# Optimization experiments

Measured on AMD Instinct MI355X. Metric: run time of the kernel, lower is better.

## Reference

```python
import jax, jax.numpy as jnp
import numpy as np
from jax import lax

N, F, V = 16, 5, 4  # batch, frames, nodes-per-frame

def _maxpool3(x):
    # MaxPool2d(kernel=3, stride=3), NCHW
    return lax.reduce_window(x, -jnp.inf, lax.max, (1, 1, 3, 3), (1, 1, 3, 3), 'VALID')

def _conv(x, w, b):
    y = lax.conv_general_dilated(x, w, window_strides=(2, 2), padding='VALID',
                                 dimension_numbers=('NCHW', 'OIHW', 'NCHW'))
    return y + b[None, :, None, None]

def setup_inputs() -> dict:
    key = jax.random.key(0)
    ks = jax.random.split(key, 24)
    s = 0.05
    inp = {
        'nodes':  jax.random.normal(ks[0], (N, F, V, 3, 224, 224), jnp.float32),
        'pos':    jax.random.normal(ks[1], (N, F, V, 6), jnp.float32),
        'attmap': jax.random.uniform(ks[2], (N, F, V, V), jnp.float32),
        'depths': jax.random.normal(ks[3], (N, F, V), jnp.float32),
        # params (linear weights stored [in, out]; y = x @ W + b)
        'conv1_w': jax.random.normal(ks[4], (3, 3, 3, 3), jnp.float32) * s,
        'conv1_b': jax.random.normal(ks[5], (3,), jnp.float32) * s,
        'conv2_w': jax.random.normal(ks[6], (1, 3, 3, 3), jnp.float32) * s,
        'conv2_b': jax.random.normal(ks[7], (1,), jnp.float32) * s,
        'lin_w':   jax.random.normal(ks[8], (36, 6), jnp.float32) * s,
        'lin_b':   jax.random.normal(ks[9], (6,), jnp.float32) * s,
        'wfc_w':   jax.random.normal(ks[10], (24, 1), jnp.float32) * s,
        'wfc_b':   jax.random.normal(ks[11], (1,), jnp.float32) * s,
        'fm_w':    jax.random.normal(ks[12], (6, 6), jnp.float32) * s,
        'fm_b':    jax.random.normal(ks[13], (6,), jnp.float32) * s,
        'lm_w':    jax.random.normal(ks[14], (6, 6), jnp.float32) * s,
        'lm_b':    jax.random.normal(ks[15], (6,), jnp.float32) * s,
        'fc1_w':   jax.random.normal(ks[16], (240, 120), jnp.float32) * s,
        'fc1_b':   jax.random.normal(ks[17], (120,), jnp.float32) * s,
        'fc2_w':   jax.random.normal(ks[18], (120, 60), jnp.float32) * s,
        'fc2_b':   jax.random.normal(ks[19], (60,), jnp.float32) * s,
        'fc3_w':   jax.random.normal(ks[20], (60, 6), jnp.float32) * s,
        'fc3_b':   jax.random.normal(ks[21], (6,), jnp.float32) * s,
    }
    return inp

def reference(nodes, pos, attmap, depths,
              conv1_w, conv1_b, conv2_w, conv2_b, lin_w, lin_b,
              wfc_w, wfc_b, fm_w, fm_b, lm_w, lm_b,
              fc1_w, fc1_b, fc2_w, fc2_b, fc3_w, fc3_b):
    # --- CNN node encoder ---
    x = nodes.reshape(N * F * V, 3, 224, 224)
    h = jax.nn.relu(_maxpool3(_conv(x, conv1_w, conv1_b)))          # [B*,3,37,37]
    h = jax.nn.relu(_maxpool3(_conv(h, conv2_w, conv2_b)))          # [B*,1,6,6]
    feat = h.reshape(N, F, V, 36) @ lin_w + lin_b                    # [N,F,V,6]

    # --- edge weights: sigmoid(W . cat(feat_src, feat_tgt)) ---
    na = jnp.concatenate([feat, pos], axis=-1)                       # [N,F,V,12]
    src = jnp.broadcast_to(na[:, :, :, None, :], (N, F, V, V, 12))   # s along axis 2
    tgt = jnp.broadcast_to(na[:, :, None, :, :], (N, F, V, V, 12))   # t along axis 3
    ef = jnp.concatenate([src, tgt], axis=-1)                        # [N,F,V,V,24]
    link = jax.nn.sigmoid((ef @ wfc_w)[..., 0] + wfc_b[0])           # [N,F,s,t]

    maw = link + attmap                                              # [N,F,s,t]

    # --- attention-weighted message aggregation over source nodes ---
    pm = pos @ fm_w + fm_b                                           # [N,F,V,6]
    agg = jnp.einsum('bfsn,bfsd->bfnd', maw, pm)                     # [N,F,V,6]

    # last-frame message (frame 0 has none)
    prev = jnp.concatenate([jnp.zeros_like(pos[:, :1]), pos[:, :-1]], axis=1)
    lm = prev @ lm_w + lm_b                                          # [N,F,V,6]
    frame_mask = (jnp.arange(F) > 0)[None, :, None, None]
    pos_up = agg + jnp.where(frame_mask, lm, 0.0)

    # --- readout MLP ---
    inp = jnp.concatenate([feat, pos_up], axis=-1).reshape(N, F * V * 12)  # [N,240]
    r = jax.nn.relu(inp @ fc1_w + fc1_b)
    r = jax.nn.relu(r @ fc2_w + fc2_b)
    return r @ fc3_w + fc3_b                                         # [N,6]
```

## Files before the change

### kernel.cpp

```cpp
#include <hip/hip_runtime.h>
#include <math.h>

#define NB 16
#define NF 5
#define NV 4
#define NIMG (NB*NF*NV)
#define IMG_HW 224
#define IMG_CH_STRIDE (224*224)
#define H1_HW 37
#define H1_CH_STRIDE (37*37)
#define H1_IMG 4108
#define PB_PER_IMG 19

typedef float v4f __attribute__((ext_vector_type(4)));

__global__ __launch_bounds__(256) void k1_conv1_pool(
    const float* __restrict__ nodes,
    const float* __restrict__ w,
    const float* __restrict__ bias,
    float* __restrict__ h1)
{
    const int blk = blockIdx.x;
    const int img = blk / PB_PER_IMG;
    const int pb  = blk - img * PB_PER_IMG;
    const int t   = threadIdx.x;

    const int py0    = 2 * pb;
    const int nrows  = (pb == PB_PER_IMG - 1) ? 1 : 2;
    const int r0     = 12 * pb;
    const int nflt   = (6 * nrows + 1) * 224;
    const int nf4    = nflt >> 2;

    __shared__ float s[3 * 13 * 224];
    __shared__ float s_w[27 * 3];
    __shared__ float s_b[3];

    if (t < 81) s_w[t] = w[t];
    if (t < 3)  s_b[t] = bias[t];

    {
        const v4f* s0 = (const v4f*)(nodes + (size_t)img * 3 * IMG_CH_STRIDE + r0 * IMG_HW);
        const v4f* s1 = s0 + (IMG_CH_STRIDE >> 2);
        const v4f* s2 = s1 + (IMG_CH_STRIDE >> 2);
        v4f* d0 = (v4f*)s;
        v4f* d1 = (v4f*)(s + nflt);
        v4f* d2 = (v4f*)(s + 2 * nflt);
        for (int i = t; i < nf4; i += 256) {
            v4f a0 = __builtin_nontemporal_load(&s0[i]);
            v4f a1 = __builtin_nontemporal_load(&s1[i]);
            v4f a2 = __builtin_nontemporal_load(&s2[i]);
            d0[i] = a0; d1[i] = a1; d2[i] = a2;
        }
    }
    __syncthreads();

    if (t < 111 * nrows) {
        const int r  = (t >= 111) ? 1 : 0;
        const int u  = t - 111 * r;
        const int oc = u / 37;
        const int px = u - 37 * oc;

        float acc[9];
        #pragma unroll
        for (int p = 0; p < 9; ++p) acc[p] = 0.f;

        #pragma unroll
        for (int ic = 0; ic < 3; ++ic) {
            float wv[9];
            #pragma unroll
            for (int k = 0; k < 9; ++k) wv[k] = s_w[(oc * 3 + ic) * 9 + k];

            float patch[7][8];
            #pragma unroll
            for (int rr = 0; rr < 7; ++rr) {
                const float* row = s + ic * nflt + (6 * r + rr) * 224 + 6 * px;
                #pragma unroll
                for (int k = 0; k < 4; ++k) {
                    float2 q = *(const float2*)(row + 2 * k);
                    patch[rr][2 * k]     = q.x;
                    patch[rr][2 * k + 1] = q.y;
                }
            }

            #pragma unroll
            for (int i = 0; i < 3; ++i)
                #pragma unroll
                for (int j = 0; j < 3; ++j) {
                    const int p = i * 3 + j;
                    #pragma unroll
                    for (int ky = 0; ky < 3; ++ky)
                        #pragma unroll
                        for (int kx = 0; kx < 3; ++kx)
                            acc[p] += wv[ky * 3 + kx] * patch[2 * i + ky][2 * j + kx];
                }
        }

        float m = -INFINITY;
        #pragma unroll
        for (int p = 0; p < 9; ++p) m = fmaxf(m, acc[p]);
        m += s_b[oc];
        m = fmaxf(m, 0.f);
        h1[(size_t)img * H1_IMG + oc * H1_CH_STRIDE + (py0 + r) * H1_HW + px] = m;
    }
}

__global__ __launch_bounds__(128) void k2_conv2_pool_lin(
    const float* __restrict__ h1,
    const float* __restrict__ w2,
    const float* __restrict__ b2,
    const float* __restrict__ lin_w,
    const float* __restrict__ lin_b,
    float* __restrict__ feat)
{
    const int img = blockIdx.x;
    const int t   = threadIdx.x;
    __shared__ float s[H1_IMG];
    __shared__ float s_h2[36];

    {
        const float4* src = (const float4*)(h1 + (size_t)img * H1_IMG);
        float4* d = (float4*)s;
        float4 v[8];
        #pragma unroll
        for (int k = 0; k < 8; ++k) v[k] = src[t + 128 * k];
        const bool hi = (t < 1027 - 1024);
        float4 v8;
        if (hi) v8 = src[t + 1024];
        #pragma unroll
        for (int k = 0; k < 8; ++k) d[t + 128 * k] = v[k];
        if (hi) d[t + 1024] = v8;
    }
    __syncthreads();

    if (t < 36) {
        const int py = t / 6, px = t - (t / 6) * 6;
        float m = -INFINITY;
        #pragma unroll
        for (int i = 0; i < 3; ++i)
            #pragma unroll
            for (int j = 0; j < 3; ++j) {
                const int oy = 3 * py + i, ox = 3 * px + j;
                float a = 0.f;
                #pragma unroll
                for (int ic = 0; ic < 3; ++ic)
                    #pragma unroll
                    for (int ky = 0; ky < 3; ++ky)
                        #pragma unroll
                        for (int kx = 0; kx < 3; ++kx)
                            a += w2[(ic * 3 + ky) * 3 + kx] *
                                 s[ic * H1_CH_STRIDE + (2 * oy + ky) * H1_HW + (2 * ox + kx)];
                m = fmaxf(m, a);
            }
        m += b2[0];
        s_h2[t] = fmaxf(m, 0.f);
    }
    __syncthreads();
    if (t < 6) {
        float a = lin_b[t];
        #pragma unroll
        for (int i = 0; i < 36; ++i) a += s_h2[i] * lin_w[i * 6 + t];
        feat[img * 6 + t] = a;
    }
}

__global__ __launch_bounds__(128) void k3_graph_mlp(
    const float* __restrict__ feat,
    const float* __restrict__ pos,
    const float* __restrict__ attmap,
    const float* __restrict__ wfc_w,
    const float* __restrict__ wfc_b,
    const float* __restrict__ fm_w,
    const float* __restrict__ fm_b,
    const float* __restrict__ lm_w,
    const float* __restrict__ lm_b,
    const float* __restrict__ fc1_w,
    const float* __restrict__ fc1_b,
    const float* __restrict__ fc2_w,
    const float* __restrict__ fc2_b,
    const float* __restrict__ fc3_w,
    const float* __restrict__ fc3_b,
    float* __restrict__ out)
{
    const int b = blockIdx.x;
    const int t = threadIdx.x;

    __shared__ float s_na[NF][NV][12];
    __shared__ float s_pm[NF][NV][6];
    __shared__ float s_maw[NF][NV][NV];
    __shared__ float s_inp[240];
    __shared__ float s_r1[120];
    __shared__ float s_r2[60];

    if (t < 120) {
        int f = t / 24;
        int v = (t / 6) % 4;
        int d = t % 6;
        float fv = feat[((b * NF + f) * NV + v) * 6 + d];
        float pv = pos[((b * NF + f) * NV + v) * 6 + d];
        s_na[f][v][d]     = fv;
        s_na[f][v][6 + d] = pv;
        s_inp[(f * NV + v) * 12 + d] = fv;
    }
    __syncthreads();

    if (t < 120) {
        int f = t / 24;
        int v = (t / 6) % 4;
        int d = t % 6;
        float a = fm_b[d];
        #pragma unroll
        for (int k = 0; k < 6; ++k) a += s_na[f][v][6 + k] * fm_w[k * 6 + d];
        s_pm[f][v][d] = a;
    }
    if (t < 80) {
        int f = t / 16;
        int sidx = (t / 4) % 4;
        int tt = t % 4;
        float x = wfc_b[0];
        #pragma unroll
        for (int k = 0; k < 12; ++k)
            x += wfc_w[k] * s_na[f][sidx][k] + wfc_w[12 + k] * s_na[f][tt][k];
        float sig = 1.f / (1.f + expf(-x));
        s_maw[f][sidx][tt] = sig + attmap[((b * NF + f) * NV + sidx) * NV + tt];
    }
    __syncthreads();

    if (t < 120) {
        int f = t / 24;
        int n = (t / 6) % 4;
        int d = t % 6;
        float a = 0.f;
        #pragma unroll
        for (int sidx = 0; sidx < 4; ++sidx) a += s_maw[f][sidx][n] * s_pm[f][sidx][d];
        if (f > 0) {
            float l = lm_b[d];
            #pragma unroll
            for (int k = 0; k < 6; ++k) l += s_na[f - 1][n][6 + k] * lm_w[k * 6 + d];
            a += l;
        }
        s_inp[(f * NV + n) * 12 + 6 + d] = a;
    }
    __syncthreads();

    if (t < 120) {
        float a = fc1_b[t];
        #pragma unroll 16
        for (int i = 0; i < 240; ++i) a += s_inp[i] * fc1_w[i * 120 + t];
        s_r1[t] = fmaxf(a, 0.f);
    }
    __syncthreads();

    if (t < 60) {
        float a = fc2_b[t];
        #pragma unroll 16
        for (int i = 0; i < 120; ++i) a += s_r1[i] * fc2_w[i * 60 + t];
        s_r2[t] = fmaxf(a, 0.f);
    }
    __syncthreads();

    if (t < 6) {
        float a = fc3_b[t];
        #pragma unroll 12
        for (int i = 0; i < 60; ++i) a += s_r2[i] * fc3_w[i * 6 + t];
        out[b * 6 + t] = a;
    }
}

extern "C" void kernel_launch(void* const* d_in, const int* in_sizes, int n_in,
                              void* d_out, int out_size, void* d_ws, size_t ws_size,
                              hipStream_t stream) {
    const float* nodes   = (const float*)d_in[0];
    const float* pos     = (const float*)d_in[1];
    const float* attmap  = (const float*)d_in[2];
    const float* conv1_w = (const float*)d_in[4];
    const float* conv1_b = (const float*)d_in[5];
    const float* conv2_w = (const float*)d_in[6];
    const float* conv2_b = (const float*)d_in[7];
    const float* lin_w   = (const float*)d_in[8];
    const float* lin_b   = (const float*)d_in[9];
    const float* wfc_w   = (const float*)d_in[10];
    const float* wfc_b   = (const float*)d_in[11];
    const float* fm_w    = (const float*)d_in[12];
    const float* fm_b    = (const float*)d_in[13];
    const float* lm_w    = (const float*)d_in[14];
    const float* lm_b    = (const float*)d_in[15];
    const float* fc1_w   = (const float*)d_in[16];
    const float* fc1_b   = (const float*)d_in[17];
    const float* fc2_w   = (const float*)d_in[18];
    const float* fc2_b   = (const float*)d_in[19];
    const float* fc3_w   = (const float*)d_in[20];
    const float* fc3_b   = (const float*)d_in[21];

    float* h1      = (float*)d_ws;
    float* feat_ws = h1 + (size_t)NIMG * H1_IMG;

    k1_conv1_pool<<<NIMG * PB_PER_IMG, 256, 0, stream>>>(nodes, conv1_w, conv1_b, h1);
    k2_conv2_pool_lin<<<NIMG, 128, 0, stream>>>(h1, conv2_w, conv2_b, lin_w, lin_b, feat_ws);
    k3_graph_mlp<<<NB, 128, 0, stream>>>(feat_ws, pos, attmap,
                                         wfc_w, wfc_b, fm_w, fm_b, lm_w, lm_b,
                                         fc1_w, fc1_b, fc2_w, fc2_b, fc3_w, fc3_b,
                                         (float*)d_out);
}
```

Baseline: 321.2 us.

## Compute all conv1 channels per thread, 3 pooled rows per block, fuse conv2 into graph kernel

Result: slower. 343.1 us (+6.8%).

```diff
diff --git a/kernel.cpp b/kernel.cpp
--- a/kernel.cpp
+++ b/kernel.cpp
@@ -10,7 +10,7 @@
 #define H1_HW 37
 #define H1_CH_STRIDE (37*37)
 #define H1_IMG 4108
-#define PB_PER_IMG 19
+#define PB_PER_IMG 13
 
 typedef float v4f __attribute__((ext_vector_type(4)));
 
@@ -25,18 +25,14 @@
     const int pb  = blk - img * PB_PER_IMG;
     const int t   = threadIdx.x;
 
-    const int py0    = 2 * pb;
-    const int nrows  = (pb == PB_PER_IMG - 1) ? 1 : 2;
-    const int r0     = 12 * pb;
+    const int last   = (pb == PB_PER_IMG - 1);
+    const int py0    = 3 * pb;
+    const int nrows  = last ? 1 : 3;
+    const int r0     = 18 * pb;
     const int nflt   = (6 * nrows + 1) * 224;
     const int nf4    = nflt >> 2;
 
-    __shared__ float s[3 * 13 * 224];
-    __shared__ float s_w[27 * 3];
-    __shared__ float s_b[3];
-
-    if (t < 81) s_w[t] = w[t];
-    if (t < 3)  s_b[t] = bias[t];
+    __shared__ float s[3 * 19 * 224];
 
     {
         const v4f* s0 = (const v4f*)(nodes + (size_t)img * 3 * IMG_CH_STRIDE + r0 * IMG_HW);
@@ -54,21 +50,24 @@
     }
     __syncthreads();
 
-    if (t < 111 * nrows) {
-        const int r  = (t >= 111) ? 1 : 0;
-        const int u  = t - 111 * r;
-        const int oc = u / 37;
-        const int px = u - 37 * oc;
-
-        float acc[9];
-        #pragma unroll
-        for (int p = 0; p < 9; ++p) acc[p] = 0.f;
+    if (t < H1_HW * nrows) {
+        const int r  = t / H1_HW;
+        const int px = t - H1_HW * r;
+
+        float acc[3][9];
+        #pragma unroll
+        for (int oc = 0; oc < 3; ++oc)
+            #pragma unroll
+            for (int p = 0; p < 9; ++p) acc[oc][p] = 0.f;
 
         #pragma unroll
         for (int ic = 0; ic < 3; ++ic) {
-            float wv[9];
-            #pragma unroll
-            for (int k = 0; k < 9; ++k) wv[k] = s_w[(oc * 3 + ic) * 9 + k];
+            float wv[3][9];
+            #pragma unroll
+            for (int oc = 0; oc < 3; ++oc)
+                #pragma unroll
+                for (int k = 0; k < 9; ++k)
+                    wv[oc][k] = w[(oc * 3 + ic) * 9 + k];
 
             float patch[7][8];
             #pragma unroll
@@ -90,81 +89,34 @@
                     #pragma unroll
                     for (int ky = 0; ky < 3; ++ky)
                         #pragma unroll
-                        for (int kx = 0; kx < 3; ++kx)
-                            acc[p] += wv[ky * 3 + kx] * patch[2 * i + ky][2 * j + kx];
+                        for (int kx = 0; kx < 3; ++kx) {
+                            float x = patch[2 * i + ky][2 * j + kx];
+                            acc[0][p] += wv[0][ky * 3 + kx] * x;
+                            acc[1][p] += wv[1][ky * 3 + kx] * x;
+                            acc[2][p] += wv[2][ky * 3 + kx] * x;
+                        }
                 }
         }
 
-        float m = -INFINITY;
-        #pragma unroll
-        for (int p = 0; p < 9; ++p) m = fmaxf(m, acc[p]);
-        m += s_b[oc];
-        m = fmaxf(m, 0.f);
-        h1[(size_t)img * H1_IMG + oc * H1_CH_STRIDE + (py0 + r) * H1_HW + px] = m;
+        float* outb = h1 + (size_t)img * H1_IMG + (py0 + r) * H1_HW + px;
+        #pragma unroll
+        for (int oc = 0; oc < 3; ++oc) {
+            float m = -INFINITY;
+            #pragma unroll
+            for (int p = 0; p < 9; ++p) m = fmaxf(m, acc[oc][p]);
+            m += bias[oc];
+            m = fmaxf(m, 0.f);
+            outb[oc * H1_CH_STRIDE] = m;
+        }
     }
 }
 
-__global__ __launch_bounds__(128) void k2_conv2_pool_lin(
+__global__ __launch_bounds__(256) void k23_feat_graph_mlp(
     const float* __restrict__ h1,
     const float* __restrict__ w2,
     const float* __restrict__ b2,
     const float* __restrict__ lin_w,
     const float* __restrict__ lin_b,
-    float* __restrict__ feat)
-{
-    const int img = blockIdx.x;
-    const int t   = threadIdx.x;
-    __shared__ float s[H1_IMG];
-    __shared__ float s_h2[36];
-
-    {
-        const float4* src = (const float4*)(h1 + (size_t)img * H1_IMG);
-        float4* d = (float4*)s;
-        float4 v[8];
-        #pragma unroll
-        for (int k = 0; k < 8; ++k) v[k] = src[t + 128 * k];
-        const bool hi = (t < 1027 - 1024);
-        float4 v8;
-        if (hi) v8 = src[t + 1024];
-        #pragma unroll
-        for (int k = 0; k < 8; ++k) d[t + 128 * k] = v[k];
-        if (hi) d[t + 1024] = v8;
-    }
-    __syncthreads();
-
-    if (t < 36) {
-        const int py = t / 6, px = t - (t / 6) * 6;
-        float m = -INFINITY;
-        #pragma unroll
-        for (int i = 0; i < 3; ++i)
-            #pragma unroll
-            for (int j = 0; j < 3; ++j) {
-                const int oy = 3 * py + i, ox = 3 * px + j;
-                float a = 0.f;
-                #pragma unroll
-                for (int ic = 0; ic < 3; ++ic)
-                    #pragma unroll
-                    for (int ky = 0; ky < 3; ++ky)
-                        #pragma unroll
-                        for (int kx = 0; kx < 3; ++kx)
-                            a += w2[(ic * 3 + ky) * 3 + kx] *
-                                 s[ic * H1_CH_STRIDE + (2 * oy + ky) * H1_HW + (2 * ox + kx)];
-                m = fmaxf(m, a);
-            }
-        m += b2[0];
-        s_h2[t] = fmaxf(m, 0.f);
-    }
-    __syncthreads();
-    if (t < 6) {
-        float a = lin_b[t];
-        #pragma unroll
-        for (int i = 0; i < 36; ++i) a += s_h2[i] * lin_w[i * 6 + t];
-        feat[img * 6 + t] = a;
-    }
-}
-
-__global__ __launch_bounds__(128) void k3_graph_mlp(
-    const float* __restrict__ feat,
     const float* __restrict__ pos,
     const float* __restrict__ attmap,
     const float* __restrict__ wfc_w,
@@ -184,6 +136,10 @@
     const int b = blockIdx.x;
     const int t = threadIdx.x;
 
+    __shared__ float s[5 * H1_IMG];
+    __shared__ float s_h2[5][36];
+    __shared__ float s_feat[20][6];
+
     __shared__ float s_na[NF][NV][12];
     __shared__ float s_pm[NF][NV][6];
     __shared__ float s_maw[NF][NV][NV];
@@ -191,11 +147,57 @@
     __shared__ float s_r1[120];
     __shared__ float s_r2[60];
 
+    for (int ph = 0; ph < 4; ++ph) {
+        const int img0 = b * 20 + ph * 5;
+        {
+            const float4* src = (const float4*)(h1 + (size_t)img0 * H1_IMG);
+            float4* d = (float4*)s;
+            for (int i = t; i < 5 * 1027; i += 256) d[i] = src[i];
+        }
+        __syncthreads();
+
+        if (t < 180) {
+            const int im = t / 36;
+            const int u  = t - im * 36;
+            const int py = u / 6, px = u - (u / 6) * 6;
+            const float* si = s + im * H1_IMG;
+            float m = -INFINITY;
+            #pragma unroll
+            for (int i = 0; i < 3; ++i)
+                #pragma unroll
+                for (int j = 0; j < 3; ++j) {
+                    const int oy = 3 * py + i, ox = 3 * px + j;
+                    float a = 0.f;
+                    #pragma unroll
+                    for (int ic = 0; ic < 3; ++ic)
+                        #pragma unroll
+                        for (int ky = 0; ky < 3; ++ky)
+                            #pragma unroll
+                            for (int kx = 0; kx < 3; ++kx)
+                                a += w2[(ic * 3 + ky) * 3 + kx] *
+                                     si[ic * H1_CH_STRIDE + (2 * oy + ky) * H1_HW + (2 * ox + kx)];
+                    m = fmaxf(m, a);
+                }
+            m += b2[0];
+            s_h2[im][u] = fmaxf(m, 0.f);
+        }
+        __syncthreads();
+
+        if (t < 30) {
+            const int im = t / 6, d = t - (t / 6) * 6;
+            float a = lin_b[d];
+            #pragma unroll
+            for (int i = 0; i < 36; ++i) a += s_h2[im][i] * lin_w[i * 6 + d];
+            s_feat[ph * 5 + im][d] = a;
+        }
+        __syncthreads();
+    }
+
     if (t < 120) {
         int f = t / 24;
         int v = (t / 6) % 4;
         int d = t % 6;
-        float fv = feat[((b * NF + f) * NV + v) * 6 + d];
+        float fv = s_feat[f * NV + v][d];
         float pv = pos[((b * NF + f) * NV + v) * 6 + d];
         s_na[f][v][d]     = fv;
         s_na[f][v][6 + d] = pv;
@@ -291,13 +293,12 @@
     const float* fc3_w   = (const float*)d_in[20];
     const float* fc3_b   = (const float*)d_in[21];
 
-    float* h1      = (float*)d_ws;
-    float* feat_ws = h1 + (size_t)NIMG * H1_IMG;
+    float* h1 = (float*)d_ws;
 
     k1_conv1_pool<<<NIMG * PB_PER_IMG, 256, 0, stream>>>(nodes, conv1_w, conv1_b, h1);
-    k2_conv2_pool_lin<<<NIMG, 128, 0, stream>>>(h1, conv2_w, conv2_b, lin_w, lin_b, feat_ws);
-    k3_graph_mlp<<<NB, 128, 0, stream>>>(feat_ws, pos, attmap,
-                                         wfc_w, wfc_b, fm_w, fm_b, lm_w, lm_b,
-                                         fc1_w, fc1_b, fc2_w, fc2_b, fc3_w, fc3_b,
-                                         (float*)d_out);
+    k23_feat_graph_mlp<<<NB, 256, 0, stream>>>(h1, conv2_w, conv2_b, lin_w, lin_b,
+                                               pos, attmap,
+                                               wfc_w, wfc_b, fm_w, fm_b, lm_w, lm_b,
+                                               fc1_w, fc1_b, fc2_w, fc2_b, fc3_w, fc3_b,
+                                               (float*)d_out);
 }
```
